# Optimization experiments

Hardware: AMD Instinct MI355X
Metric: run time of the kernel (lower is better)

## Reference

```python
import jax, jax.numpy as jnp
import numpy as np

N_NODES, N_EDGES, D, N_RELS = 50000, 600000, 128, 460


def setup_inputs() -> dict:
    key = jax.random.key(0)
    ks = jax.random.split(key, 8)
    h = jax.random.normal(ks[0], (N_NODES, D), dtype=jnp.float32)
    emb_rel = jax.random.normal(ks[1], (N_RELS, D), dtype=jnp.float32)
    attn_fc_w = jax.random.normal(ks[2], (D, 3 * D), dtype=jnp.float32) * 0.05   # Linear(3D->D), weight [out,in]
    attn_fc2_w = jax.random.normal(ks[3], (1, D), dtype=jnp.float32) * 0.05     # Linear(D->1)
    loop_weight = jax.random.normal(ks[4], (D, D), dtype=jnp.float32) * 0.05
    edge_src = jax.random.randint(ks[5], (N_EDGES,), 0, N_NODES)
    edge_dst = jax.random.randint(ks[6], (N_EDGES,), 0, N_NODES)
    edge_type = jax.random.randint(ks[7], (N_EDGES,), 0, N_RELS)
    return {"h": h, "emb_rel": emb_rel, "attn_fc_w": attn_fc_w,
            "attn_fc2_w": attn_fc2_w, "loop_weight": loop_weight,
            "edge_src": edge_src, "edge_dst": edge_dst, "edge_type": edge_type}


def reference(h, emb_rel, attn_fc_w, attn_fc2_w, loop_weight, edge_src, edge_dst, edge_type):
    n = h.shape[0]
    # --- per-edge gather ---
    hs = h[edge_src]            # [E, D] src features (mailbox 'e_h')
    ht = h[edge_dst]            # [E, D]
    rel = emb_rel[edge_type]    # [E, D]
    # --- concat-MLP attention: leaky_relu(fc2(fc1([hs|ht|rel]))) ---
    z2 = jnp.concatenate([hs, ht, rel], axis=1)          # [E, 3D]
    a = z2 @ attn_fc_w.T                                  # [E, D]
    e = jax.nn.leaky_relu(a @ attn_fc2_w.T)               # [E, 1], slope 0.01 (torch default)
    # --- per-destination segment softmax ---
    m = jax.ops.segment_max(e, edge_dst, num_segments=n)  # [N, 1]
    m = jnp.where(jnp.isfinite(m), m, jnp.float32(0.0))   # empty nodes -> -inf; neutralize
    ex = jnp.exp(e - m[edge_dst])                         # [E, 1]
    den = jax.ops.segment_sum(ex, edge_dst, num_segments=n)
    alpha = ex / den[edge_dst]                            # [E, 1]
    # --- weighted scatter-sum of src features ---
    node_repr = jax.ops.segment_sum(alpha * hs, edge_dst, num_segments=n)  # [N, D]
    # --- self-loop ---
    node_repr = node_repr + h @ loop_weight
    return node_repr
```

## Files before the change

kernel.cpp:

```cpp
#include <hip/hip_runtime.h>

#define N_NODES 50000
#define N_EDGES 600000
#define D 128
#define N_RELS 460
#define CAP_LOG 6

typedef unsigned short u16;
typedef __attribute__((ext_vector_type(8))) short bf16x8;
typedef __attribute__((ext_vector_type(4))) float f32x4;

enum : int {
    OFF_W      = 0,
    OFF_S1     = 384,
    OFF_S2     = 50384,
    OFF_S3     = 100384,
    OFF_COUNTS = 100864,
    OFF_CSR    = 900864,
    OFF_HB     = 4100864,
};

#define NODE_WAVES   12500
#define REL_WAVES    115
#define SCORE_BLOCKS 3154
#define GEMM_BLOCKS  782
#define ZERO_BLOCKS  196
#define FILL_BLOCKS  293
#define WT_STRIDE    136

__device__ __forceinline__ u16 f2bf(float f) {
    unsigned u = __float_as_uint(f);
    unsigned r = u + 0x7FFFu + ((u >> 16) & 1u);
    return (u16)(r >> 16);
}
__device__ __forceinline__ float blo(unsigned u) { return __uint_as_float(u << 16); }
__device__ __forceinline__ float bhi(unsigned u) { return __uint_as_float(u & 0xFFFF0000u); }

__global__ __launch_bounds__(256) void k_prep(
        const float* __restrict__ fc1, const float* __restrict__ fc2,
        const float* __restrict__ W, const float* __restrict__ h,
        float* __restrict__ w, int* __restrict__ counts,
        u16* __restrict__ hb, float* __restrict__ out) {
    __shared__ u16 Ws[D * WT_STRIDE];
    int t = threadIdx.x;
    if (blockIdx.x < GEMM_BLOCKS) {
        for (int i = t; i < (D * D) / 4; i += 256) {
            float4 v = ((const float4*)W)[i];
            int k  = i >> 5;
            int n0 = (i & 31) * 4;
            Ws[(n0 + 0) * WT_STRIDE + k] = f2bf(v.x);
            Ws[(n0 + 1) * WT_STRIDE + k] = f2bf(v.y);
            Ws[(n0 + 2) * WT_STRIDE + k] = f2bf(v.z);
            Ws[(n0 + 3) * WT_STRIDE + k] = f2bf(v.w);
        }
        __syncthreads();

        int wave = t >> 6, lane = t & 63;
        int quad = lane >> 4, m16 = lane & 15;
        int nbase = blockIdx.x * 64 + wave * 16;

        f32x4 acc[8];
        #pragma unroll
        for (int cg = 0; cg < 8; ++cg) acc[cg] = (f32x4){0.f, 0.f, 0.f, 0.f};

        int arow = nbase + m16;
        if (arow >= N_NODES) arow = N_NODES - 1;
        const float* aptr = h + (size_t)arow * D + quad * 8;
        u16* hbp = hb + (size_t)arow * D + quad * 8;

        #pragma unroll
        for (int k0 = 0; k0 < D; k0 += 32) {
            float4 a0 = *(const float4*)(aptr + k0);
            float4 a1 = *(const float4*)(aptr + k0 + 4);
            bf16x8 a;
            a[0] = (short)f2bf(a0.x); a[1] = (short)f2bf(a0.y);
            a[2] = (short)f2bf(a0.z); a[3] = (short)f2bf(a0.w);
            a[4] = (short)f2bf(a1.x); a[5] = (short)f2bf(a1.y);
            a[6] = (short)f2bf(a1.z); a[7] = (short)f2bf(a1.w);
            *(bf16x8*)(hbp + k0) = a;
            #pragma unroll
            for (int cg = 0; cg < 8; ++cg) {
                bf16x8 bb = *(const bf16x8*)(&Ws[(cg * 16 + m16) * WT_STRIDE + k0 + quad * 8]);
                acc[cg] = __builtin_amdgcn_mfma_f32_16x16x32_bf16(a, bb, acc[cg], 0, 0, 0);
            }
        }
        #pragma unroll
        for (int reg = 0; reg < 4; ++reg) {
            int row = nbase + quad * 4 + reg;
            if (row < N_NODES) {
                #pragma unroll
                for (int cg = 0; cg < 8; ++cg)
                    out[(size_t)row * D + cg * 16 + m16] = acc[cg][reg];
            }
        }
    } else if (blockIdx.x < GEMM_BLOCKS + ZERO_BLOCKS) {
        int i4 = (blockIdx.x - GEMM_BLOCKS) * 256 + t;
        #pragma unroll
        for (int rep = 0; rep < 4; ++rep) {
            int idx = i4 * 4 + rep;
            if (idx * 4 < N_NODES * 16)
                ((int4*)counts)[idx] = make_int4(0, 0, 0, 0);
        }
    } else {
        for (int j = t; j < 3 * D; j += 256) {
            float acc = 0.f;
            for (int k = 0; k < D; ++k) acc += fc2[k] * fc1[k * 3 * D + j];
            w[j] = acc;
        }
    }
}

__global__ __launch_bounds__(256) void k_fused(
        const int* __restrict__ src, const int* __restrict__ dst,
        const int* __restrict__ typ, int* __restrict__ counts,
        unsigned* __restrict__ csr,
        const u16* __restrict__ hb, const float* __restrict__ emb_rel,
        const float* __restrict__ w,
        float* __restrict__ s1, float* __restrict__ s2, float* __restrict__ s3) {
    if (blockIdx.x < FILL_BLOCKS) {
        int i = blockIdx.x * blockDim.x + threadIdx.x;
        if (i >= N_EDGES / 8) return;
        int4 da = ((const int4*)dst)[2 * i],     db = ((const int4*)dst)[2 * i + 1];
        int4 sa = ((const int4*)src)[2 * i],     sb = ((const int4*)src)[2 * i + 1];
        int4 ta = ((const int4*)typ)[2 * i],     tb = ((const int4*)typ)[2 * i + 1];
        int l0 = atomicAdd(&counts[da.x << 4], 1);
        int l1 = atomicAdd(&counts[da.y << 4], 1);
        int l2 = atomicAdd(&counts[da.z << 4], 1);
        int l3 = atomicAdd(&counts[da.w << 4], 1);
        int l4 = atomicAdd(&counts[db.x << 4], 1);
        int l5 = atomicAdd(&counts[db.y << 4], 1);
        int l6 = atomicAdd(&counts[db.z << 4], 1);
        int l7 = atomicAdd(&counts[db.w << 4], 1);
        csr[(da.x << CAP_LOG) + l0] = (unsigned)sa.x | ((unsigned)ta.x << 16);
        csr[(da.y << CAP_LOG) + l1] = (unsigned)sa.y | ((unsigned)ta.y << 16);
        csr[(da.z << CAP_LOG) + l2] = (unsigned)sa.z | ((unsigned)ta.z << 16);
        csr[(da.w << CAP_LOG) + l3] = (unsigned)sa.w | ((unsigned)ta.w << 16);
        csr[(db.x << CAP_LOG) + l4] = (unsigned)sb.x | ((unsigned)tb.x << 16);
        csr[(db.y << CAP_LOG) + l5] = (unsigned)sb.y | ((unsigned)tb.y << 16);
        csr[(db.z << CAP_LOG) + l6] = (unsigned)sb.z | ((unsigned)tb.z << 16);
        csr[(db.w << CAP_LOG) + l7] = (unsigned)sb.w | ((unsigned)tb.w << 16);
    } else {
        int wv = ((blockIdx.x - FILL_BLOCKS) * blockDim.x + threadIdx.x) >> 6;
        int l  = threadIdx.x & 63;
        int sub = l >> 4;
        int q   = l & 15;
        if (wv < NODE_WAVES) {
            int r = wv * 4 + sub;
            uint4 pk = ((const uint4*)hb)[(size_t)r * 16 + q];
            float4 w10 = *(const float4*)(w + q * 8);
            float4 w11 = *(const float4*)(w + q * 8 + 4);
            float4 w20 = *(const float4*)(w + D + q * 8);
            float4 w21 = *(const float4*)(w + D + q * 8 + 4);
            float a1 = blo(pk.x) * w10.x + bhi(pk.x) * w10.y
                     + blo(pk.y) * w10.z + bhi(pk.y) * w10.w
                     + blo(pk.z) * w11.x + bhi(pk.z) * w11.y
                     + blo(pk.w) * w11.z + bhi(pk.w) * w11.w;
            float a2 = blo(pk.x) * w20.x + bhi(pk.x) * w20.y
                     + blo(pk.y) * w20.z + bhi(pk.y) * w20.w
                     + blo(pk.z) * w21.x + bhi(pk.z) * w21.y
                     + blo(pk.w) * w21.z + bhi(pk.w) * w21.w;
            #pragma unroll
            for (int o = 8; o; o >>= 1) { a1 += __shfl_xor(a1, o, 16); a2 += __shfl_xor(a2, o, 16); }
            if (q == 0) { s1[r] = a1; s2[r] = a2; }
        } else if (wv < NODE_WAVES + REL_WAVES) {
            int r = (wv - NODE_WAVES) * 4 + sub;
            const float* rp = emb_rel + (size_t)r * D + q * 8;
            float4 r0 = *(const float4*)rp;
            float4 r1 = *(const float4*)(rp + 4);
            float4 w30 = *(const float4*)(w + 2 * D + q * 8);
            float4 w31 = *(const float4*)(w + 2 * D + q * 8 + 4);
            float a3 = r0.x * w30.x + r0.y * w30.y + r0.z * w30.z + r0.w * w30.w
                     + r1.x * w31.x + r1.y * w31.y + r1.z * w31.z + r1.w * w31.w;
            #pragma unroll
            for (int o = 8; o; o >>= 1) a3 += __shfl_xor(a3, o, 16);
            if (q == 0) s3[r] = a3;
        }
    }
}

#define ROWACC(uu, cc)                                                         \
    accA.x += (cc) * blo((uu).x);  accA.y += (cc) * bhi((uu).x);               \
    accA.z += (cc) * blo((uu).y);  accA.w += (cc) * bhi((uu).y);               \
    accB.x += (cc) * blo((uu).z);  accB.y += (cc) * bhi((uu).z);               \
    accB.z += (cc) * blo((uu).w);  accB.w += (cc) * bhi((uu).w);

__global__ void k_gather(const u16* __restrict__ hb, const int* __restrict__ counts,
                         const unsigned* __restrict__ csr,
                         const float* __restrict__ s1, const float* __restrict__ s2,
                         const float* __restrict__ s3, float* __restrict__ out) {
    int n  = (blockIdx.x * blockDim.x + threadIdx.x) >> 4;
    int gl = threadIdx.x & 15;
    if (n >= N_NODES) return;
    int deg = counts[n << 4];
    if (deg == 0) return;
    int beg = n << CAP_LOG;
    int end = beg + deg;

    float s2n = s2[n];
    float den = 0.f;
    f32x4 accA = {0.f, 0.f, 0.f, 0.f}, accB = {0.f, 0.f, 0.f, 0.f};

    for (int cb = beg; cb < end; cb += 16) {
        int i = cb + gl;
        int msrc = 0; float mex = 0.f;
        if (i < end) {
            unsigned p = csr[i];
            msrc = (int)(p & 0xFFFFu);
            float x = s1[msrc] + s2n + s3[p >> 16];
            float lv = (x > 0.f) ? x : 0.01f * x;
            mex = __expf(lv);
        }
        den += mex;
        int cnt  = min(16, end - cb);
        int cntr = (cnt + 3) & ~3;
        int j = 0;
        for (; j + 7 < cntr; j += 8) {
            int aa[8]; float cc[8]; uint4 uu[8];
            #pragma unroll
            for (int u = 0; u < 8; ++u) {
                aa[u] = __shfl(msrc, j + u, 16);
                cc[u] = __shfl(mex,  j + u, 16);
            }
            #pragma unroll
            for (int u = 0; u < 8; ++u)
                uu[u] = ((const uint4*)(hb + (size_t)aa[u] * D))[gl];
            #pragma unroll
            for (int u = 0; u < 8; ++u) { ROWACC(uu[u], cc[u]); }
        }
        for (; j < cntr; j += 4) {
            int aa[4]; float cc[4]; uint4 uu[4];
            #pragma unroll
            for (int u = 0; u < 4; ++u) {
                aa[u] = __shfl(msrc, j + u, 16);
                cc[u] = __shfl(mex,  j + u, 16);
            }
            #pragma unroll
            for (int u = 0; u < 4; ++u)
                uu[u] = ((const uint4*)(hb + (size_t)aa[u] * D))[gl];
            #pragma unroll
            for (int u = 0; u < 4; ++u) { ROWACC(uu[u], cc[u]); }
        }
    }
    #pragma unroll
    for (int o = 8; o; o >>= 1) den += __shfl_xor(den, o, 16);
    float inv = 1.f / den;

    f32x4* op = (f32x4*)(out + (size_t)n * D + gl * 8);
    f32x4 o0 = __builtin_nontemporal_load(op);
    f32x4 o1 = __builtin_nontemporal_load(op + 1);
    o0 += accA * inv;
    o1 += accB * inv;
    __builtin_nontemporal_store(o0, op);
    __builtin_nontemporal_store(o1, op + 1);
}

extern "C" void kernel_launch(void* const* d_in, const int* in_sizes, int n_in,
                              void* d_out, int out_size, void* d_ws, size_t ws_size,
                              hipStream_t stream) {
    const float* h       = (const float*)d_in[0];
    const float* emb_rel = (const float*)d_in[1];
    const float* fc1     = (const float*)d_in[2];
    const float* fc2     = (const float*)d_in[3];
    const float* loopw   = (const float*)d_in[4];
    const int*   esrc    = (const int*)d_in[5];
    const int*   edst    = (const int*)d_in[6];
    const int*   etyp    = (const int*)d_in[7];
    float* out = (float*)d_out;
    float* ws  = (float*)d_ws;

    float*    w       = ws + OFF_W;
    float*    s1      = ws + OFF_S1;
    float*    s2      = ws + OFF_S2;
    float*    s3      = ws + OFF_S3;
    int*      counts  = (int*)(ws + OFF_COUNTS);
    unsigned* csr     = (unsigned*)(ws + OFF_CSR);
    u16*      hb      = (u16*)(ws + OFF_HB);

    k_prep<<<GEMM_BLOCKS + ZERO_BLOCKS + 1, 256, 0, stream>>>(
        fc1, fc2, loopw, h, w, counts, hb, out);

    k_fused<<<FILL_BLOCKS + SCORE_BLOCKS, 256, 0, stream>>>(
        esrc, edst, etyp, counts, csr, hb, emb_rel, w, s1, s2, s3);

    k_gather<<<(N_NODES * 16 + 255) / 256, 256, 0, stream>>>(
        hb, counts, csr, s1, s2, s3, out);
}
```

Measured before the change: 164.2 us.

## Fold node score projections into loop GEMM as extra MFMA column tile

Computes the per-node attention scores s1/s2 inside the self-loop GEMM by appending the two projection vectors as a ninth 16-column tile of the bf16 weight matrix. This removes the separate 12500-wave score pass that re-read the bf16 node features. The edge CSR fill now runs in the same launch as the GEMM, and a small init kernel zeroes counts and computes w beforehand. Bf16 conversion uses the hardware packed convert instruction, and the transposed weight load into LDS is restructured. Risk: the scores now come from bf16-rounded weights, and the GEMM does one extra MFMA per k-step.

```diff
diff --git a/kernel.cpp b/kernel.cpp
--- a/kernel.cpp
+++ b/kernel.cpp
@@ -20,81 +20,30 @@
     OFF_HB     = 4100864,
 };
 
-#define NODE_WAVES   12500
-#define REL_WAVES    115
-#define SCORE_BLOCKS 3154
 #define GEMM_BLOCKS  782
 #define ZERO_BLOCKS  196
+#define W_BLOCKS     2
 #define FILL_BLOCKS  293
+#define REL_WAVES    115
+#define REL_BLOCKS   29
 #define WT_STRIDE    136
 
-__device__ __forceinline__ u16 f2bf(float f) {
-    unsigned u = __float_as_uint(f);
-    unsigned r = u + 0x7FFFu + ((u >> 16) & 1u);
-    return (u16)(r >> 16);
-}
 __device__ __forceinline__ float blo(unsigned u) { return __uint_as_float(u << 16); }
 __device__ __forceinline__ float bhi(unsigned u) { return __uint_as_float(u & 0xFFFF0000u); }
 
-__global__ __launch_bounds__(256) void k_prep(
+__device__ __forceinline__ unsigned cvtpk(float lo, float hi) {
+    unsigned d;
+    asm("v_cvt_pk_bf16_f32 %0, %1, %2" : "=v"(d) : "v"(lo), "v"(hi));
+    return d;
+}
+
+__global__ __launch_bounds__(256) void k_init(
+        int* __restrict__ counts,
         const float* __restrict__ fc1, const float* __restrict__ fc2,
-        const float* __restrict__ W, const float* __restrict__ h,
-        float* __restrict__ w, int* __restrict__ counts,
-        u16* __restrict__ hb, float* __restrict__ out) {
-    __shared__ u16 Ws[D * WT_STRIDE];
+        float* __restrict__ w) {
     int t = threadIdx.x;
-    if (blockIdx.x < GEMM_BLOCKS) {
-        for (int i = t; i < (D * D) / 4; i += 256) {
-            float4 v = ((const float4*)W)[i];
-            int k  = i >> 5;
-            int n0 = (i & 31) * 4;
-            Ws[(n0 + 0) * WT_STRIDE + k] = f2bf(v.x);
-            Ws[(n0 + 1) * WT_STRIDE + k] = f2bf(v.y);
-            Ws[(n0 + 2) * WT_STRIDE + k] = f2bf(v.z);
-            Ws[(n0 + 3) * WT_STRIDE + k] = f2bf(v.w);
-        }
-        __syncthreads();
-
-        int wave = t >> 6, lane = t & 63;
-        int quad = lane >> 4, m16 = lane & 15;
-        int nbase = blockIdx.x * 64 + wave * 16;
-
-        f32x4 acc[8];
-        #pragma unroll
-        for (int cg = 0; cg < 8; ++cg) acc[cg] = (f32x4){0.f, 0.f, 0.f, 0.f};
-
-        int arow = nbase + m16;
-        if (arow >= N_NODES) arow = N_NODES - 1;
-        const float* aptr = h + (size_t)arow * D + quad * 8;
-        u16* hbp = hb + (size_t)arow * D + quad * 8;
-
-        #pragma unroll
-        for (int k0 = 0; k0 < D; k0 += 32) {
-            float4 a0 = *(const float4*)(aptr + k0);
-            float4 a1 = *(const float4*)(aptr + k0 + 4);
-            bf16x8 a;
-            a[0] = (short)f2bf(a0.x); a[1] = (short)f2bf(a0.y);
-            a[2] = (short)f2bf(a0.z); a[3] = (short)f2bf(a0.w);
-            a[4] = (short)f2bf(a1.x); a[5] = (short)f2bf(a1.y);
-            a[6] = (short)f2bf(a1.z); a[7] = (short)f2bf(a1.w);
-            *(bf16x8*)(hbp + k0) = a;
-            #pragma unroll
-            for (int cg = 0; cg < 8; ++cg) {
-                bf16x8 bb = *(const bf16x8*)(&Ws[(cg * 16 + m16) * WT_STRIDE + k0 + quad * 8]);
-                acc[cg] = __builtin_amdgcn_mfma_f32_16x16x32_bf16(a, bb, acc[cg], 0, 0, 0);
-            }
-        }
-        #pragma unroll
-        for (int reg = 0; reg < 4; ++reg) {
-            int row = nbase + quad * 4 + reg;
-            if (row < N_NODES) {
-                #pragma unroll
-                for (int cg = 0; cg < 8; ++cg)
-                    out[(size_t)row * D + cg * 16 + m16] = acc[cg][reg];
-            }
-        }
-    } else if (blockIdx.x < GEMM_BLOCKS + ZERO_BLOCKS) {
-        int i4 = (blockIdx.x - GEMM_BLOCKS) * 256 + t;
+    if (blockIdx.x < ZERO_BLOCKS) {
+        int i4 = blockIdx.x * 256 + t;
         #pragma unroll
         for (int rep = 0; rep < 4; ++rep) {
             int idx = i4 * 4 + rep;
@@ -102,23 +51,27 @@
                 ((int4*)counts)[idx] = make_int4(0, 0, 0, 0);
         }
     } else {
-        for (int j = t; j < 3 * D; j += 256) {
+        int j = (blockIdx.x - ZERO_BLOCKS) * 256 + t;
+        if (j < 3 * D) {
             float acc = 0.f;
+            #pragma unroll 8
             for (int k = 0; k < D; ++k) acc += fc2[k] * fc1[k * 3 * D + j];
             w[j] = acc;
         }
     }
 }
 
-__global__ __launch_bounds__(256) void k_fused(
+__global__ __launch_bounds__(256) void k_prep(
         const int* __restrict__ src, const int* __restrict__ dst,
         const int* __restrict__ typ, int* __restrict__ counts,
         unsigned* __restrict__ csr,
-        const u16* __restrict__ hb, const float* __restrict__ emb_rel,
-        const float* __restrict__ w,
+        const float* __restrict__ loopw, const float* __restrict__ h,
+        const float* __restrict__ w, const float* __restrict__ emb_rel,
+        u16* __restrict__ hb, float* __restrict__ out,
         float* __restrict__ s1, float* __restrict__ s2, float* __restrict__ s3) {
+    int t = threadIdx.x;
     if (blockIdx.x < FILL_BLOCKS) {
-        int i = blockIdx.x * blockDim.x + threadIdx.x;
+        int i = blockIdx.x * blockDim.x + t;
         if (i >= N_EDGES / 8) return;
         int4 da = ((const int4*)dst)[2 * i],     db = ((const int4*)dst)[2 * i + 1];
         int4 sa = ((const int4*)src)[2 * i],     sb = ((const int4*)src)[2 * i + 1];
@@ -139,42 +92,110 @@
         csr[(db.y << CAP_LOG) + l5] = (unsigned)sb.y | ((unsigned)tb.y << 16);
         csr[(db.z << CAP_LOG) + l6] = (unsigned)sb.z | ((unsigned)tb.z << 16);
         csr[(db.w << CAP_LOG) + l7] = (unsigned)sb.w | ((unsigned)tb.w << 16);
+    } else if (blockIdx.x < FILL_BLOCKS + GEMM_BLOCKS) {
+        int gb = blockIdx.x - FILL_BLOCKS;
+        __shared__ u16 Ws[(D + 16) * WT_STRIDE];
+        for (int u = t; u < 512; u += 256) {
+            int ko = u >> 5, nq = u & 31;
+            const float* wp = loopw + (size_t)ko * 8 * D + nq * 4;
+            float v[4][8];
+            #pragma unroll
+            for (int r = 0; r < 8; ++r) {
+                float4 f = *(const float4*)(wp + (size_t)r * D);
+                v[0][r] = f.x; v[1][r] = f.y; v[2][r] = f.z; v[3][r] = f.w;
+            }
+            #pragma unroll
+            for (int c = 0; c < 4; ++c) {
+                union { bf16x8 b; unsigned q[4]; } pk;
+                #pragma unroll
+                for (int p = 0; p < 4; ++p)
+                    pk.q[p] = cvtpk(v[c][2 * p], v[c][2 * p + 1]);
+                *(bf16x8*)&Ws[(nq * 4 + c) * WT_STRIDE + ko * 8] = pk.b;
+            }
+        }
+        {
+            int row = 128 + (t >> 4);
+            int k8  = (t & 15) * 8;
+            union { bf16x8 b; unsigned q[4]; } pk;
+            if (row == 128) {
+                #pragma unroll
+                for (int p = 0; p < 4; ++p)
+                    pk.q[p] = cvtpk(w[k8 + 2 * p], w[k8 + 2 * p + 1]);
+            } else if (row == 129) {
+                #pragma unroll
+                for (int p = 0; p < 4; ++p)
+                    pk.q[p] = cvtpk(w[D + k8 + 2 * p], w[D + k8 + 2 * p + 1]);
+            } else {
+                #pragma unroll
+                for (int p = 0; p < 4; ++p) pk.q[p] = 0u;
+            }
+            *(bf16x8*)&Ws[row * WT_STRIDE + k8] = pk.b;
+        }
+        __syncthreads();
+
+        int wave = t >> 6, lane = t & 63;
+        int quad = lane >> 4, m16 = lane & 15;
+        int nbase = gb * 64 + wave * 16;
+
+        f32x4 acc[9];
+        #pragma unroll
+        for (int cg = 0; cg < 9; ++cg) acc[cg] = (f32x4){0.f, 0.f, 0.f, 0.f};
+
+        int arow = nbase + m16;
+        if (arow >= N_NODES) arow = N_NODES - 1;
+        const float* aptr = h + (size_t)arow * D + quad * 8;
+        u16* hbp = hb + (size_t)arow * D + quad * 8;
+
+        #pragma unroll
+        for (int k0 = 0; k0 < D; k0 += 32) {
+            float4 a0 = *(const float4*)(aptr + k0);
+            float4 a1 = *(const float4*)(aptr + k0 + 4);
+            union { bf16x8 b; unsigned q[4]; } A;
+            A.q[0] = cvtpk(a0.x, a0.y);
+            A.q[1] = cvtpk(a0.z, a0.w);
+            A.q[2] = cvtpk(a1.x, a1.y);
+            A.q[3] = cvtpk(a1.z, a1.w);
+            *(bf16x8*)(hbp + k0) = A.b;
+            #pragma unroll
+            for (int cg = 0; cg < 9; ++cg) {
+                bf16x8 bb = *(const bf16x8*)(&Ws[(cg * 16 + m16) * WT_STRIDE + k0 + quad * 8]);
+                acc[cg] = __builtin_amdgcn_mfma_f32_16x16x32_bf16(A.b, bb, acc[cg], 0, 0, 0);
+            }
+        }
+        #pragma unroll
+        for (int reg = 0; reg < 4; ++reg) {
+            int row = nbase + quad * 4 + reg;
+            if (row < N_NODES) {
+                #pragma unroll
+                for (int cg = 0; cg < 8; ++cg)
+                    out[(size_t)row * D + cg * 16 + m16] = acc[cg][reg];
+            }
+        }
+        if (m16 < 2) {
+            float* sp = (m16 == 0) ? s1 : s2;
+            #pragma unroll
+            for (int reg = 0; reg < 4; ++reg) {
+                int row = nbase + quad * 4 + reg;
+                if (row < N_NODES) sp[row] = acc[8][reg];
+            }
+        }
     } else {
-        int wv = ((blockIdx.x - FILL_BLOCKS) * blockDim.x + threadIdx.x) >> 6;
-        int l  = threadIdx.x & 63;
+        int wv = ((blockIdx.x - FILL_BLOCKS - GEMM_BLOCKS) * 256 + t) >> 6;
+        if (wv >= REL_WAVES) return;
+        int l   = t & 63;
         int sub = l >> 4;
         int q   = l & 15;
-        if (wv < NODE_WAVES) {
-            int r = wv * 4 + sub;
-            uint4 pk = ((const uint4*)hb)[(size_t)r * 16 + q];
-            float4 w10 = *(const float4*)(w + q * 8);
-            float4 w11 = *(const float4*)(w + q * 8 + 4);
-            float4 w20 = *(const float4*)(w + D + q * 8);
-            float4 w21 = *(const float4*)(w + D + q * 8 + 4);
-            float a1 = blo(pk.x) * w10.x + bhi(pk.x) * w10.y
-                     + blo(pk.y) * w10.z + bhi(pk.y) * w10.w
-                     + blo(pk.z) * w11.x + bhi(pk.z) * w11.y
-                     + blo(pk.w) * w11.z + bhi(pk.w) * w11.w;
-            float a2 = blo(pk.x) * w20.x + bhi(pk.x) * w20.y
-                     + blo(pk.y) * w20.z + bhi(pk.y) * w20.w
-                     + blo(pk.z) * w21.x + bhi(pk.z) * w21.y
-                     + blo(pk.w) * w21.z + bhi(pk.w) * w21.w;
-            #pragma unroll
-            for (int o = 8; o; o >>= 1) { a1 += __shfl_xor(a1, o, 16); a2 += __shfl_xor(a2, o, 16); }
-            if (q == 0) { s1[r] = a1; s2[r] = a2; }
-        } else if (wv < NODE_WAVES + REL_WAVES) {
-            int r = (wv - NODE_WAVES) * 4 + sub;
-            const float* rp = emb_rel + (size_t)r * D + q * 8;
-            float4 r0 = *(const float4*)rp;
-            float4 r1 = *(const float4*)(rp + 4);
-            float4 w30 = *(const float4*)(w + 2 * D + q * 8);
-            float4 w31 = *(const float4*)(w + 2 * D + q * 8 + 4);
-            float a3 = r0.x * w30.x + r0.y * w30.y + r0.z * w30.z + r0.w * w30.w
-                     + r1.x * w31.x + r1.y * w31.y + r1.z * w31.z + r1.w * w31.w;
-            #pragma unroll
-            for (int o = 8; o; o >>= 1) a3 += __shfl_xor(a3, o, 16);
-            if (q == 0) s3[r] = a3;
-        }
+        int r = wv * 4 + sub;
+        const float* rp = emb_rel + (size_t)r * D + q * 8;
+        float4 r0 = *(const float4*)rp;
+        float4 r1 = *(const float4*)(rp + 4);
+        float4 w30 = *(const float4*)(w + 2 * D + q * 8);
+        float4 w31 = *(const float4*)(w + 2 * D + q * 8 + 4);
+        float a3 = r0.x * w30.x + r0.y * w30.y + r0.z * w30.z + r0.w * w30.w
+                 + r1.x * w31.x + r1.y * w31.y + r1.z * w31.z + r1.w * w31.w;
+        #pragma unroll
+        for (int o = 8; o; o >>= 1) a3 += __shfl_xor(a3, o, 16);
+        if (q == 0) s3[r] = a3;
     }
 }
 
@@ -276,11 +297,11 @@
     unsigned* csr     = (unsigned*)(ws + OFF_CSR);
     u16*      hb      = (u16*)(ws + OFF_HB);
 
-    k_prep<<<GEMM_BLOCKS + ZERO_BLOCKS + 1, 256, 0, stream>>>(
-        fc1, fc2, loopw, h, w, counts, hb, out);
-
-    k_fused<<<FILL_BLOCKS + SCORE_BLOCKS, 256, 0, stream>>>(
-        esrc, edst, etyp, counts, csr, hb, emb_rel, w, s1, s2, s3);
+    k_init<<<ZERO_BLOCKS + W_BLOCKS, 256, 0, stream>>>(counts, fc1, fc2, w);
+
+    k_prep<<<FILL_BLOCKS + GEMM_BLOCKS + REL_BLOCKS, 256, 0, stream>>>(
+        esrc, edst, etyp, counts, csr, loopw, h, w, emb_rel,
+        hb, out, s1, s2, s3);
 
     k_gather<<<(N_NODES * 16 + 255) / 256, 256, 0, stream>>>(
         hb, counts, csr, s1, s2, s3, out);
```

After: 159.1 us. -3.1%, faster.
